# Kernel tuning notes

Measured on AMD Instinct MI355X. Metric: run time of the kernel, lower is better.

Reference implementation:

```python
import math
import jax, jax.numpy as jnp
import numpy as np

BLOCKSIZE = 1024  # Hadamard block length (power of 2, divides in_features=4096)


def fwht(x):
    """Fast Walsh-Hadamard transform over the last dim (power of 2), unnormalized.
    Iterative butterfly: H_{2h} = [[H_h, H_h], [H_h, -H_h]]."""
    n = x.shape[-1]
    steps = int(math.log2(n))
    shape = x.shape
    x = x.reshape(-1, n)
    h = 1
    for _ in range(steps):
        x = x.reshape(-1, n // (2 * h), 2, h)
        a = x[:, :, 0, :]
        b = x[:, :, 1, :]
        x = jnp.stack([a + b, a - b], axis=2).reshape(-1, n)
        h *= 2
    return x.reshape(shape)


def pad_to_block_last(x, blocksize):
    size = x.shape[-1]
    target = ((size - 1) // blocksize + 1) * blocksize
    delta = target - size
    if delta == 0:
        return x
    pad = [(0, 0)] * (x.ndim - 1) + [(0, delta)]
    return jnp.pad(x, pad)


def setup_inputs() -> dict:
    key = jax.random.key(0)
    k1, k2 = jax.random.split(key)
    x = jax.random.normal(k1, (4, 2048, 4096), dtype=jnp.float32)
    # HadLinear.__init__ divides the weight by sqrt(blocksize) when do_hadamard=True;
    # the stored parameter is the scaled weight, so we materialize it scaled.
    w = jax.random.normal(k2, (4096, 4096), dtype=jnp.float32) / math.sqrt(BLOCKSIZE)
    return {"input": x, "weight": w}


def reference(input, weight):
    bs = BLOCKSIZE
    x = pad_to_block_last(input, bs)
    lead = x.shape[:-1]
    d = x.shape[-1]
    mult = d // bs
    x = x.reshape(lead + (mult, bs))
    x = fwht(x) * (1.0 / math.sqrt(bs))  # hadamard_transform with scale=1/sqrt(bs)
    x = x.reshape(lead + (d,))
    return jnp.einsum('bsd,od->bso', x, weight)  # F.linear(x, weight)
```

## Files before the change

### kernel.cpp

```cpp
#include <hip/hip_runtime.h>
#include <hip/hip_bf16.h>
#include <cstdint>

typedef __attribute__((ext_vector_type(4))) float f32x4;
typedef __attribute__((ext_vector_type(8))) short bf16x8;
typedef unsigned short u16;

__device__ inline u16 f2b(float f) {
    union { float f; uint32_t u; } c; c.f = f;
    uint32_t r = (c.u + 0x7FFFu + ((c.u >> 16) & 1u)) >> 16;
    return (u16)r;
}

__global__ void cast_x_kernel(const float4* __restrict__ X, ushort4* __restrict__ Xb, int n4) {
    int i = blockIdx.x * blockDim.x + threadIdx.x;
    int stride = gridDim.x * blockDim.x;
    for (; i < n4; i += stride) {
        float4 v = X[i];
        ushort4 o;
        o.x = f2b(v.x); o.y = f2b(v.y); o.z = f2b(v.z); o.w = f2b(v.w);
        Xb[i] = o;
    }
}

__global__ void fwht_w_kernel(const float* __restrict__ W, u16* __restrict__ Wh) {
    __shared__ float s[1024];
    const float* src = W + (size_t)blockIdx.x * 1024;
    for (int i = threadIdx.x; i < 1024; i += 256) s[i] = src[i];
    __syncthreads();
    for (int h = 1; h < 1024; h <<= 1) {
        for (int p = threadIdx.x; p < 512; p += 256) {
            int i = ((p & ~(h - 1)) << 1) | (p & (h - 1));
            float a = s[i], b = s[i + h];
            s[i] = a + b;
            s[i + h] = a - b;
        }
        __syncthreads();
    }
    u16* dst = Wh + (size_t)blockIdx.x * 1024;
    for (int i = threadIdx.x; i < 1024; i += 256) dst[i] = f2b(s[i] * 0.03125f);
}

#define MFMA16(a, b, c) __builtin_amdgcn_mfma_f32_16x16x32_bf16(a, b, c, 0, 0, 0)

__global__ __launch_bounds__(512) void gemm256_kernel(
    const u16* __restrict__ A, const u16* __restrict__ B, float* __restrict__ C,
    int M, int N, int K)
{
    __shared__ u16 lds[2][2][2][8192];

    const int tid  = threadIdx.x;
    const int wid  = tid >> 6;
    const int lane = tid & 63;
    const int wr   = wid >> 2;
    const int wc   = wid & 3;

    const int ntn = N / 256;
    const int nwg = (M / 256) * ntn;
    int bid = blockIdx.x;
    int swz = (nwg % 8 == 0) ? ((bid & 7) * (nwg >> 3) + (bid >> 3)) : bid;
    const int tm = swz / ntn, tn = swz % ntn;
    const size_t rowA0 = (size_t)tm * 256;
    const size_t rowB0 = (size_t)tn * 256;
    const int TSTEPS = K / 64;

    const int stg_row  = wid * 8 + (lane >> 3);
    const int stg_slot = (lane & 7) ^ (stg_row & 7);

    const int frow = (lane & 15) * 64;
    const int fs0  = (((lane >> 4)) ^ (lane & 7)) * 8;
    const int fs1  = ((4 + (lane >> 4)) ^ (lane & 7)) * 8;

    auto stage = [&](const u16* __restrict__ G, size_t rowbase, u16* ldsHalf, int chunk, int t) {
        int teff = t < TSTEPS ? t : TSTEPS - 1;
        const u16* g = G + (rowbase + (size_t)(chunk * 64 + stg_row)) * (size_t)K
                         + teff * 64 + stg_slot * 8;
        u16* l = ldsHalf + chunk * 4096 + wid * 512;
        __builtin_amdgcn_global_load_lds((const __attribute__((address_space(1))) void*)g,
                                         (__attribute__((address_space(3))) void*)l, 16, 0, 0);
    };

    f32x4 acc[8][4];
#pragma unroll
    for (int i = 0; i < 8; ++i)
#pragma unroll
        for (int j = 0; j < 4; ++j) acc[i][j] = (f32x4)(0.0f);

    bf16x8 aR[4][2], b0R[2][2], b1R[2][2];

    stage(A, rowA0,       &lds[0][0][0][0], 0, 0);
    stage(A, rowA0,       &lds[0][0][0][0], 1, 0);
    stage(B, rowB0,       &lds[0][1][0][0], 0, 0);
    stage(B, rowB0,       &lds[0][1][0][0], 1, 0);
    stage(A, rowA0 + 128, &lds[0][0][1][0], 0, 0);
    stage(A, rowA0 + 128, &lds[0][0][1][0], 1, 0);
    stage(B, rowB0 + 128, &lds[0][1][1][0], 0, 0);
    stage(B, rowB0 + 128, &lds[0][1][1][0], 1, 0);
    stage(B, rowB0,       &lds[1][1][0][0], 0, 1);
    stage(B, rowB0,       &lds[1][1][0][0], 1, 1);
    stage(A, rowA0,       &lds[1][0][0][0], 0, 1);
    stage(A, rowA0,       &lds[1][0][0][0], 1, 1);
    stage(A, rowA0 + 128, &lds[1][0][1][0], 0, 1);
    stage(A, rowA0 + 128, &lds[1][0][1][0], 1, 1);
    asm volatile("s_waitcnt vmcnt(6)" ::: "memory");
    __builtin_amdgcn_s_barrier();

    for (int t = 0; t < TSTEPS; ++t) {
        const int cb = t & 1, nb = cb ^ 1;
        const u16* Ahalf = &lds[cb][0][wr][0];
        const u16* Bbase = &lds[cb][1][wc >> 1][(wc & 1) * 4096];

#pragma unroll
        for (int i = 0; i < 4; ++i) {
            aR[i][0] = *(const bf16x8*)&Ahalf[i * 1024 + frow + fs0];
            aR[i][1] = *(const bf16x8*)&Ahalf[i * 1024 + frow + fs1];
        }
#pragma unroll
        for (int j = 0; j < 2; ++j) {
            b0R[j][0] = *(const bf16x8*)&Bbase[j * 1024 + frow + fs0];
            b0R[j][1] = *(const bf16x8*)&Bbase[j * 1024 + frow + fs1];
        }
        stage(B, rowB0 + 128, &lds[nb][1][1][0], 0, t + 1);
        stage(B, rowB0 + 128, &lds[nb][1][1][0], 1, t + 1);
        __builtin_amdgcn_s_barrier();
        asm volatile("s_waitcnt lgkmcnt(0)" ::: "memory");
        __builtin_amdgcn_s_setprio(1);
#pragma unroll
        for (int i = 0; i < 4; ++i)
#pragma unroll
            for (int j = 0; j < 2; ++j) {
                acc[i][j] = MFMA16(aR[i][0], b0R[j][0], acc[i][j]);
                acc[i][j] = MFMA16(aR[i][1], b0R[j][1], acc[i][j]);
            }
        __builtin_amdgcn_s_setprio(0);
        __builtin_amdgcn_s_barrier();

#pragma unroll
        for (int j = 0; j < 2; ++j) {
            b1R[j][0] = *(const bf16x8*)&Bbase[(2 + j) * 1024 + frow + fs0];
            b1R[j][1] = *(const bf16x8*)&Bbase[(2 + j) * 1024 + frow + fs1];
        }
        __builtin_amdgcn_s_barrier();
        asm volatile("s_waitcnt lgkmcnt(0)" ::: "memory");
        __builtin_amdgcn_s_setprio(1);
#pragma unroll
        for (int i = 0; i < 4; ++i)
#pragma unroll
            for (int j = 0; j < 2; ++j) {
                acc[i][2 + j] = MFMA16(aR[i][0], b1R[j][0], acc[i][2 + j]);
                acc[i][2 + j] = MFMA16(aR[i][1], b1R[j][1], acc[i][2 + j]);
            }
        __builtin_amdgcn_s_setprio(0);
        __builtin_amdgcn_s_barrier();

#pragma unroll
        for (int i = 0; i < 4; ++i) {
            aR[i][0] = *(const bf16x8*)&Ahalf[(4 + i) * 1024 + frow + fs0];
            aR[i][1] = *(const bf16x8*)&Ahalf[(4 + i) * 1024 + frow + fs1];
        }
        stage(B, rowB0, &lds[cb][1][0][0], 0, t + 2);
        stage(B, rowB0, &lds[cb][1][0][0], 1, t + 2);
        __builtin_amdgcn_s_barrier();
        asm volatile("s_waitcnt lgkmcnt(0)" ::: "memory");
        __builtin_amdgcn_s_setprio(1);
#pragma unroll
        for (int i = 0; i < 4; ++i)
#pragma unroll
            for (int j = 0; j < 2; ++j) {
                acc[4 + i][2 + j] = MFMA16(aR[i][0], b1R[j][0], acc[4 + i][2 + j]);
                acc[4 + i][2 + j] = MFMA16(aR[i][1], b1R[j][1], acc[4 + i][2 + j]);
            }
        __builtin_amdgcn_s_setprio(0);
        __builtin_amdgcn_s_barrier();

        stage(A, rowA0,       &lds[cb][0][0][0], 0, t + 2);
        stage(A, rowA0,       &lds[cb][0][0][0], 1, t + 2);
        stage(A, rowA0 + 128, &lds[cb][0][1][0], 0, t + 2);
        stage(A, rowA0 + 128, &lds[cb][0][1][0], 1, t + 2);
        asm volatile("s_waitcnt vmcnt(6)" ::: "memory");
        __builtin_amdgcn_s_barrier();
        __builtin_amdgcn_s_setprio(1);
#pragma unroll
        for (int i = 0; i < 4; ++i)
#pragma unroll
            for (int j = 0; j < 2; ++j) {
                acc[4 + i][j] = MFMA16(aR[i][0], b0R[j][0], acc[4 + i][j]);
                acc[4 + i][j] = MFMA16(aR[i][1], b0R[j][1], acc[4 + i][j]);
            }
        __builtin_amdgcn_s_setprio(0);
        __builtin_amdgcn_s_barrier();
    }

#pragma unroll
    for (int mf = 0; mf < 8; ++mf) {
        size_t row = rowA0 + wr * 128 + mf * 16 + (lane >> 4) * 4;
#pragma unroll
        for (int nf = 0; nf < 4; ++nf) {
            size_t col = rowB0 + wc * 64 + nf * 16 + (lane & 15);
            f32x4 v = acc[mf][nf];
#pragma unroll
            for (int j = 0; j < 4; ++j)
                C[(row + j) * (size_t)N + col] = v[j];
        }
    }
}

extern "C" void kernel_launch(void* const* d_in, const int* in_sizes, int n_in,
                              void* d_out, int out_size, void* d_ws, size_t ws_size,
                              hipStream_t stream) {
    const float* X = (const float*)d_in[0];
    const float* W = (const float*)d_in[1];
    float* Out = (float*)d_out;

    const int K = 4096;
    const int N = in_sizes[1] / K;
    const int M = in_sizes[0] / K;

    u16* Xb = (u16*)d_ws;
    u16* Wh = (u16*)d_ws + (size_t)M * K;

    cast_x_kernel<<<2048, 256, 0, stream>>>((const float4*)X, (ushort4*)Xb, (M * K) / 4);
    fwht_w_kernel<<<(size_t)N * K / 1024, 256, 0, stream>>>(W, Wh);

    dim3 grid((M / 256) * (N / 256));
    gemm256_kernel<<<grid, 512, 0, stream>>>(Xb, Wh, Out, M, N, K);
}
```

Baseline: 316.6 us.

## Split GEMM k-step into half-K phases with fewer operand registers

The main loop is reordered so each 64-wide k-step runs as four phases. Each phase uses one 32-wide K half (fs0, then fs1) against all four B fragments, instead of holding both K halves for half the B fragments. This roughly halves the live A/B fragment registers, and launch bounds now ask for two blocks per CU. Global staging is moved to overlap with the final MFMA phases. The risks are more LDS read rounds per k-step, and the 128KB LDS footprint per block may still rule out a second resident block.

```diff
diff --git a/kernel.cpp b/kernel.cpp
--- a/kernel.cpp
+++ b/kernel.cpp
@@ -43,7 +43,7 @@
 
 #define MFMA16(a, b, c) __builtin_amdgcn_mfma_f32_16x16x32_bf16(a, b, c, 0, 0, 0)
 
-__global__ __launch_bounds__(512) void gemm256_kernel(
+__global__ __launch_bounds__(512, 2) void gemm256_kernel(
     const u16* __restrict__ A, const u16* __restrict__ B, float* __restrict__ C,
     int M, int N, int K)
 {
@@ -85,8 +85,6 @@
     for (int i = 0; i < 8; ++i)
 #pragma unroll
         for (int j = 0; j < 4; ++j) acc[i][j] = (f32x4)(0.0f);
-
-    bf16x8 aR[4][2], b0R[2][2], b1R[2][2];
 
     stage(A, rowA0,       &lds[0][0][0][0], 0, 0);
     stage(A, rowA0,       &lds[0][0][0][0], 1, 0);
@@ -110,16 +108,12 @@
         const u16* Ahalf = &lds[cb][0][wr][0];
         const u16* Bbase = &lds[cb][1][wc >> 1][(wc & 1) * 4096];
 
-#pragma unroll
-        for (int i = 0; i < 4; ++i) {
-            aR[i][0] = *(const bf16x8*)&Ahalf[i * 1024 + frow + fs0];
-            aR[i][1] = *(const bf16x8*)&Ahalf[i * 1024 + frow + fs1];
-        }
-#pragma unroll
-        for (int j = 0; j < 2; ++j) {
-            b0R[j][0] = *(const bf16x8*)&Bbase[j * 1024 + frow + fs0];
-            b0R[j][1] = *(const bf16x8*)&Bbase[j * 1024 + frow + fs1];
-        }
+        bf16x8 aCur[4], bCur[4];
+
+#pragma unroll
+        for (int i = 0; i < 4; ++i) aCur[i] = *(const bf16x8*)&Ahalf[i * 1024 + frow + fs0];
+#pragma unroll
+        for (int j = 0; j < 4; ++j) bCur[j] = *(const bf16x8*)&Bbase[j * 1024 + frow + fs0];
         stage(B, rowB0 + 128, &lds[nb][1][1][0], 0, t + 1);
         stage(B, rowB0 + 128, &lds[nb][1][1][0], 1, t + 1);
         __builtin_amdgcn_s_barrier();
@@ -128,66 +122,59 @@
 #pragma unroll
         for (int i = 0; i < 4; ++i)
 #pragma unroll
-            for (int j = 0; j < 2; ++j) {
-                acc[i][j] = MFMA16(aR[i][0], b0R[j][0], acc[i][j]);
-                acc[i][j] = MFMA16(aR[i][1], b0R[j][1], acc[i][j]);
-            }
-        __builtin_amdgcn_s_setprio(0);
-        __builtin_amdgcn_s_barrier();
-
-#pragma unroll
-        for (int j = 0; j < 2; ++j) {
-            b1R[j][0] = *(const bf16x8*)&Bbase[(2 + j) * 1024 + frow + fs0];
-            b1R[j][1] = *(const bf16x8*)&Bbase[(2 + j) * 1024 + frow + fs1];
-        }
-        __builtin_amdgcn_s_barrier();
-        asm volatile("s_waitcnt lgkmcnt(0)" ::: "memory");
-        __builtin_amdgcn_s_setprio(1);
-#pragma unroll
-        for (int i = 0; i < 4; ++i)
-#pragma unroll
-            for (int j = 0; j < 2; ++j) {
-                acc[i][2 + j] = MFMA16(aR[i][0], b1R[j][0], acc[i][2 + j]);
-                acc[i][2 + j] = MFMA16(aR[i][1], b1R[j][1], acc[i][2 + j]);
-            }
-        __builtin_amdgcn_s_setprio(0);
-        __builtin_amdgcn_s_barrier();
-
-#pragma unroll
-        for (int i = 0; i < 4; ++i) {
-            aR[i][0] = *(const bf16x8*)&Ahalf[(4 + i) * 1024 + frow + fs0];
-            aR[i][1] = *(const bf16x8*)&Ahalf[(4 + i) * 1024 + frow + fs1];
-        }
+            for (int j = 0; j < 4; ++j)
+                acc[i][j] = MFMA16(aCur[i], bCur[j], acc[i][j]);
+        __builtin_amdgcn_s_setprio(0);
+        __builtin_amdgcn_s_barrier();
+
+#pragma unroll
+        for (int i = 0; i < 4; ++i) aCur[i] = *(const bf16x8*)&Ahalf[(4 + i) * 1024 + frow + fs0];
+        __builtin_amdgcn_s_barrier();
+        asm volatile("s_waitcnt lgkmcnt(0)" ::: "memory");
+        __builtin_amdgcn_s_setprio(1);
+#pragma unroll
+        for (int i = 0; i < 4; ++i)
+#pragma unroll
+            for (int j = 0; j < 4; ++j)
+                acc[4 + i][j] = MFMA16(aCur[i], bCur[j], acc[4 + i][j]);
+        __builtin_amdgcn_s_setprio(0);
+        __builtin_amdgcn_s_barrier();
+
+#pragma unroll
+        for (int i = 0; i < 4; ++i) aCur[i] = *(const bf16x8*)&Ahalf[i * 1024 + frow + fs1];
+#pragma unroll
+        for (int j = 0; j < 4; ++j) bCur[j] = *(const bf16x8*)&Bbase[j * 1024 + frow + fs1];
+        __builtin_amdgcn_s_barrier();
+        asm volatile("s_waitcnt lgkmcnt(0)" ::: "memory");
+        __builtin_amdgcn_sched_barrier(0);
         stage(B, rowB0, &lds[cb][1][0][0], 0, t + 2);
         stage(B, rowB0, &lds[cb][1][0][0], 1, t + 2);
-        __builtin_amdgcn_s_barrier();
-        asm volatile("s_waitcnt lgkmcnt(0)" ::: "memory");
-        __builtin_amdgcn_s_setprio(1);
-#pragma unroll
-        for (int i = 0; i < 4; ++i)
-#pragma unroll
-            for (int j = 0; j < 2; ++j) {
-                acc[4 + i][2 + j] = MFMA16(aR[i][0], b1R[j][0], acc[4 + i][2 + j]);
-                acc[4 + i][2 + j] = MFMA16(aR[i][1], b1R[j][1], acc[4 + i][2 + j]);
-            }
-        __builtin_amdgcn_s_setprio(0);
-        __builtin_amdgcn_s_barrier();
-
+        __builtin_amdgcn_s_setprio(1);
+#pragma unroll
+        for (int i = 0; i < 4; ++i)
+#pragma unroll
+            for (int j = 0; j < 4; ++j)
+                acc[i][j] = MFMA16(aCur[i], bCur[j], acc[i][j]);
+        __builtin_amdgcn_s_setprio(0);
+        __builtin_amdgcn_s_barrier();
+
+#pragma unroll
+        for (int i = 0; i < 4; ++i) aCur[i] = *(const bf16x8*)&Ahalf[(4 + i) * 1024 + frow + fs1];
+        __builtin_amdgcn_s_barrier();
+        asm volatile("s_waitcnt lgkmcnt(0)" ::: "memory");
+        __builtin_amdgcn_sched_barrier(0);
         stage(A, rowA0,       &lds[cb][0][0][0], 0, t + 2);
         stage(A, rowA0,       &lds[cb][0][0][0], 1, t + 2);
         stage(A, rowA0 + 128, &lds[cb][0][1][0], 0, t + 2);
         stage(A, rowA0 + 128, &lds[cb][0][1][0], 1, t + 2);
+        __builtin_amdgcn_s_setprio(1);
+#pragma unroll
+        for (int i = 0; i < 4; ++i)
+#pragma unroll
+            for (int j = 0; j < 4; ++j)
+                acc[4 + i][j] = MFMA16(aCur[i], bCur[j], acc[4 + i][j]);
+        __builtin_amdgcn_s_setprio(0);
         asm volatile("s_waitcnt vmcnt(6)" ::: "memory");
-        __builtin_amdgcn_s_barrier();
-        __builtin_amdgcn_s_setprio(1);
-#pragma unroll
-        for (int i = 0; i < 4; ++i)
-#pragma unroll
-            for (int j = 0; j < 2; ++j) {
-                acc[4 + i][j] = MFMA16(aR[i][0], b0R[j][0], acc[4 + i][j]);
-                acc[4 + i][j] = MFMA16(aR[i][1], b0R[j][1], acc[4 + i][j]);
-            }
-        __builtin_amdgcn_s_setprio(0);
         __builtin_amdgcn_s_barrier();
     }
 
```

Measured after the change: 317.7 us. Within noise of the previous version (+0.4%).
